# Performance work log

Hardware: AMD Instinct MI355X
Metric: run time of the kernel (lower is better)

The kernel has to match this reference:

```python
import jax, jax.numpy as jnp
import numpy as np

NUM_SEGMENTS = 64  # number of bags (max batch id + 1)
TEMP = 1.0
EPS_NORM = 1e-12
EPS_SOFTMAX = 1e-16

D = 1024
L = 128
N = 262144


def setup_inputs() -> dict:
    key = jax.random.key(0)
    ks = jax.random.split(key, 8)
    feature = jax.random.normal(ks[0], (N, D), dtype=jnp.float32)
    batch = jnp.sort(jax.random.randint(ks[1], (N,), 0, NUM_SEGMENTS, dtype=jnp.int32))
    # xavier_normal_ init: std = sqrt(2/(fan_in+fan_out))
    Wa = jax.random.normal(ks[2], (L, D), dtype=jnp.float32) * np.sqrt(2.0 / (D + L))
    ba = jnp.zeros((L,), dtype=jnp.float32)
    Wb = jax.random.normal(ks[3], (L, D), dtype=jnp.float32) * np.sqrt(2.0 / (D + L))
    bb = jnp.zeros((L,), dtype=jnp.float32)
    Wc = jax.random.normal(ks[4], (1, L), dtype=jnp.float32) * np.sqrt(2.0 / (L + 1))
    bc = jnp.zeros((1,), dtype=jnp.float32)
    return {"feature": feature, "batch": batch, "istrain": 0,
            "Wa": Wa, "ba": ba, "Wb": Wb, "bb": bb, "Wc": Wc, "bc": bc}


def segment_softmax(score, batch, num_segments):
    # score: [N, 1], batch: [N] segment ids (torch_geometric softmax semantics)
    seg_max = jax.ops.segment_max(score, batch, num_segments=num_segments)
    ex = jnp.exp(score - seg_max[batch])
    denom = jax.ops.segment_sum(ex, batch, num_segments=num_segments)
    return ex / (denom[batch] + EPS_SOFTMAX)


def reference(feature, batch, istrain, Wa, ba, Wb, bb, Wc, bc):
    # F.normalize: L2-normalize each row (dim=1)
    norm = jnp.linalg.norm(feature, axis=1, keepdims=True)
    instance_norm_feature = feature / jnp.maximum(norm, EPS_NORM)
    a = jax.nn.sigmoid(feature @ Wa.T + ba)          # [N, L]
    b = jnp.tanh(feature @ Wb.T + bb)                # [N, L]
    gated = a * b                                     # [N, L]
    score = (gated @ Wc.T + bc) / TEMP               # [N, 1]
    score = segment_softmax(score, batch, NUM_SEGMENTS)
    # istrain=0 -> dropout is identity in this reference
    return (instance_norm_feature, score)
```

## Files before the change

kernel.cpp:

```cpp
#include <hip/hip_runtime.h>

#define DD 1024
#define LL 128
#define NSEG 64
#define CHS 544
#define TB  17408
#define GRID 768
#define NTILE 16384

typedef float floatx4 __attribute__((ext_vector_type(4)));

__global__ __launch_bounds__(256)
void prep_kernel(const float* __restrict__ Wa, const float* __restrict__ Wb,
                 unsigned char* __restrict__ Wf8, float* __restrict__ denom,
                 float* __restrict__ score_raw)
{
    int gid = blockIdx.x * 256 + threadIdx.x;
    if (gid < 2 * LL * DD) {
        const int j    = gid & 7;
        const int lane = (gid >> 3) & 63;
        const int ct   = (gid >> 9) & 15;
        const int c    = gid >> 13;
        const int r = ct * 16 + (lane & 15);
        const int k = c * 32 + (lane >> 4) * 8 + j;
        const float v = ((r < LL) ? Wa[r * DD + k] : Wb[(r - LL) * DD + k]) * 16.0f;
        unsigned u = __builtin_amdgcn_cvt_pk_fp8_f32(v, v, 0, false);
        Wf8[gid] = (unsigned char)(u & 0xFF);
        score_raw[gid] = 0.0f;
    }
    if (gid < NSEG) denom[gid] = 0.0f;
}

__global__ __launch_bounds__(512, 6)
void fused_main(const float* __restrict__ feat,
                const unsigned char* __restrict__ Wf8,
                const float* __restrict__ ba,
                const float* __restrict__ bb,
                const float* __restrict__ Wc,
                float* __restrict__ out_norm,
                float* __restrict__ score_raw)
{
    __shared__ __align__(16) char tile[2 * TB];

    const int tid  = threadIdx.x;
    const int wave = tid >> 6;
    const int lane = tid & 63;
    const int s15  = lane & 15;
    const int l4   = lane >> 4;

    const float bav = ba[wave * 16 + s15];
    const float bbv = bb[wave * 16 + s15];
    const float wcv = Wc[wave * 16 + s15];
    const unsigned char* bb0 = Wf8 + (size_t)wave * 512 + (size_t)lane * 8;

    float4 L[2][4];

    auto issue = [&](long long T) {
        const float* fb = feat + ((size_t)T * 16 + wave * 2) * DD + lane * 4;
        #pragma unroll
        for (int i = 0; i < 2; ++i)
            #pragma unroll
            for (int c = 0; c < 4; ++c)
                L[i][c] = *reinterpret_cast<const float4*>(fb + (size_t)i * DD + c * 256);
    };

    long long t = blockIdx.x;
    int parity = 0;
    if (t < NTILE) issue(t);

    while (t < NTILE) {
        const long long row0 = t * 16;
        char* tb = tile + parity * TB;

        unsigned pw[2][4];
        #pragma unroll
        for (int i = 0; i < 2; ++i) {
            float ss = 0.0f;
            #pragma unroll
            for (int c = 0; c < 4; ++c)
                ss += L[i][c].x * L[i][c].x + L[i][c].y * L[i][c].y
                    + L[i][c].z * L[i][c].z + L[i][c].w * L[i][c].w;
            #pragma unroll
            for (int off = 32; off >= 1; off >>= 1) ss += __shfl_xor(ss, off);
            const float rinv = 1.0f / fmaxf(sqrtf(ss), 1e-12f);

            float* ob = out_norm + (row0 + wave * 2 + i) * DD + lane * 4;
            #pragma unroll
            for (int c = 0; c < 4; ++c) {
                float4 v;
                v.x = L[i][c].x * rinv; v.y = L[i][c].y * rinv;
                v.z = L[i][c].z * rinv; v.w = L[i][c].w * rinv;
                *reinterpret_cast<float4*>(ob + c * 256) = v;
            }
            #pragma unroll
            for (int c = 0; c < 4; ++c) {
                unsigned u = __builtin_amdgcn_cvt_pk_fp8_f32(L[i][c].x * 8.0f, L[i][c].y * 8.0f, 0, false);
                u = __builtin_amdgcn_cvt_pk_fp8_f32(L[i][c].z * 8.0f, L[i][c].w * 8.0f, u, true);
                pw[i][c] = u;
            }
        }

        #pragma unroll
        for (int i = 0; i < 2; ++i) {
            const int r = wave * 2 + i;
            #pragma unroll
            for (int c = 0; c < 4; ++c) {
                const int chunk = (lane >> 3) + c * 8;
                const int addr  = parity * TB + chunk * CHS + r * 32 + ((lane >> 1) & 3) * 8 + (lane & 1) * 4;
                *reinterpret_cast<unsigned*>(tile + addr) = pw[i][c];
            }
        }

        const long long tn = t + GRID;
        if (tn < NTILE) issue(tn);
        __builtin_amdgcn_sched_barrier(0);

        __syncthreads();

        floatx4 acc0 = (floatx4)0.0f;
        floatx4 acc1 = (floatx4)0.0f;
        #pragma unroll 4
        for (int c = 0; c < 32; ++c) {
            const long long a8 = *reinterpret_cast<const long long*>(tb + c * CHS + s15 * 32 + l4 * 8);
            const long long w0 = *reinterpret_cast<const long long*>(bb0 + (size_t)c * 8192);
            const long long w1 = *reinterpret_cast<const long long*>(bb0 + (size_t)c * 8192 + 4096);
            acc0 = __builtin_amdgcn_mfma_f32_16x16x32_fp8_fp8(a8, w0, acc0, 0, 0, 0);
            acc1 = __builtin_amdgcn_mfma_f32_16x16x32_fp8_fp8(a8, w1, acc1, 0, 0, 0);
        }

        {
            const float S = 1.0f / 128.0f;
            float s[4];
            #pragma unroll
            for (int j = 0; j < 4; ++j) {
                const float av = 1.0f / (1.0f + expf(-(acc0[j] * S + bav)));
                const float bv = tanhf(acc1[j] * S + bbv);
                s[j] = av * bv * wcv;
            }
            #pragma unroll
            for (int j = 0; j < 4; ++j) {
                s[j] += __shfl_xor(s[j], 1);
                s[j] += __shfl_xor(s[j], 2);
                s[j] += __shfl_xor(s[j], 4);
                s[j] += __shfl_xor(s[j], 8);
            }
            if (s15 == 0) {
                #pragma unroll
                for (int j = 0; j < 4; ++j)
                    atomicAdd(&score_raw[row0 + l4 * 4 + j], s[j]);
            }
        }

        t = tn;
        parity ^= 1;
    }
}

__global__ __launch_bounds__(256)
void seg_exp_kernel(float* __restrict__ score_inout, const int* __restrict__ batch,
                    float* __restrict__ denom, int n)
{
    __shared__ float sd[NSEG];
    const int t = threadIdx.x;
    if (t < NSEG) sd[t] = 0.0f;
    __syncthreads();
    const int stride = gridDim.x * blockDim.x;
    for (int i = blockIdx.x * blockDim.x + t; i < n; i += stride) {
        const float e = expf(score_inout[i]);
        score_inout[i] = e;
        atomicAdd(&sd[batch[i]], e);
    }
    __syncthreads();
    if (t < NSEG) atomicAdd(&denom[t], sd[t]);
}

__global__ __launch_bounds__(256)
void seg_div_kernel(float* __restrict__ score_inout, const int* __restrict__ batch,
                    const float* __restrict__ denom, int n)
{
    const int stride = gridDim.x * blockDim.x;
    for (int i = blockIdx.x * blockDim.x + threadIdx.x; i < n; i += stride)
        score_inout[i] = score_inout[i] / (denom[batch[i]] + 1e-16f);
}

extern "C" void kernel_launch(void* const* d_in, const int* in_sizes, int n_in,
                              void* d_out, int out_size, void* d_ws, size_t ws_size,
                              hipStream_t stream)
{
    const float* feat  = (const float*)d_in[0];
    const int*   batch = (const int*)d_in[1];
    const float* Wa = (const float*)d_in[3];
    const float* ba = (const float*)d_in[4];
    const float* Wb = (const float*)d_in[5];
    const float* bb = (const float*)d_in[6];
    const float* Wc = (const float*)d_in[7];

    const int N = in_sizes[1];

    float* out_norm  = (float*)d_out;
    float* out_score = (float*)d_out + (size_t)N * DD;

    char* ws = (char*)d_ws;
    unsigned char* Wf8 = (unsigned char*)ws;
    float* denom = (float*)(ws + 2 * LL * DD);

    prep_kernel<<<(2 * LL * DD + 255) / 256, 256, 0, stream>>>(Wa, Wb, Wf8, denom, out_score);
    fused_main<<<GRID, 512, 0, stream>>>(feat, Wf8, ba, bb, Wc, out_norm, out_score);
    seg_exp_kernel<<<512, 256, 0, stream>>>(out_score, batch, denom, N);
    seg_div_kernel<<<512, 256, 0, stream>>>(out_score, batch, denom, N);
}
```

Before: 546.4 us.

## Fuse segment softmax kernels with grid barrier, nontemporal loads, fast math

Merges the exp/sum and divide segment-softmax kernels into one launch that waits on a global atomic counter as a grid-wide barrier, removing one kernel launch. The main kernel now loads features with nontemporal hints and issues the next tile's loads before the LDS stores. It also swaps expf/tanhf for __expf-based sigmoid and tanh. The spin barrier relies on all 256 blocks being co-resident, and the exp-based tanh can overflow to inf/inf for large inputs.

```diff
diff --git a/kernel.cpp b/kernel.cpp
--- a/kernel.cpp
+++ b/kernel.cpp
@@ -7,13 +7,15 @@
 #define TB  17408
 #define GRID 768
 #define NTILE 16384
+#define SGRID 256
 
 typedef float floatx4 __attribute__((ext_vector_type(4)));
+typedef float f4v __attribute__((ext_vector_type(4)));
 
 __global__ __launch_bounds__(256)
 void prep_kernel(const float* __restrict__ Wa, const float* __restrict__ Wb,
                  unsigned char* __restrict__ Wf8, float* __restrict__ denom,
-                 float* __restrict__ score_raw)
+                 unsigned* __restrict__ counter, float* __restrict__ score_raw)
 {
     int gid = blockIdx.x * 256 + threadIdx.x;
     if (gid < 2 * LL * DD) {
@@ -29,6 +31,7 @@
         score_raw[gid] = 0.0f;
     }
     if (gid < NSEG) denom[gid] = 0.0f;
+    if (gid == NSEG) *counter = 0u;
 }
 
 __global__ __launch_bounds__(512, 6)
@@ -53,7 +56,7 @@
     const float wcv = Wc[wave * 16 + s15];
     const unsigned char* bb0 = Wf8 + (size_t)wave * 512 + (size_t)lane * 8;
 
-    float4 L[2][4];
+    f4v L[2][4];
 
     auto issue = [&](long long T) {
         const float* fb = feat + ((size_t)T * 16 + wave * 2) * DD + lane * 4;
@@ -61,7 +64,8 @@
         for (int i = 0; i < 2; ++i)
             #pragma unroll
             for (int c = 0; c < 4; ++c)
-                L[i][c] = *reinterpret_cast<const float4*>(fb + (size_t)i * DD + c * 256);
+                L[i][c] = __builtin_nontemporal_load(
+                    reinterpret_cast<const f4v*>(fb + (size_t)i * DD + c * 256));
     };
 
     long long t = blockIdx.x;
@@ -78,8 +82,8 @@
             float ss = 0.0f;
             #pragma unroll
             for (int c = 0; c < 4; ++c)
-                ss += L[i][c].x * L[i][c].x + L[i][c].y * L[i][c].y
-                    + L[i][c].z * L[i][c].z + L[i][c].w * L[i][c].w;
+                ss += L[i][c][0]*L[i][c][0] + L[i][c][1]*L[i][c][1]
+                    + L[i][c][2]*L[i][c][2] + L[i][c][3]*L[i][c][3];
             #pragma unroll
             for (int off = 32; off >= 1; off >>= 1) ss += __shfl_xor(ss, off);
             const float rinv = 1.0f / fmaxf(sqrtf(ss), 1e-12f);
@@ -87,18 +91,21 @@
             float* ob = out_norm + (row0 + wave * 2 + i) * DD + lane * 4;
             #pragma unroll
             for (int c = 0; c < 4; ++c) {
-                float4 v;
-                v.x = L[i][c].x * rinv; v.y = L[i][c].y * rinv;
-                v.z = L[i][c].z * rinv; v.w = L[i][c].w * rinv;
-                *reinterpret_cast<float4*>(ob + c * 256) = v;
+                f4v v;
+                v[0] = L[i][c][0] * rinv; v[1] = L[i][c][1] * rinv;
+                v[2] = L[i][c][2] * rinv; v[3] = L[i][c][3] * rinv;
+                *reinterpret_cast<f4v*>(ob + c * 256) = v;
             }
             #pragma unroll
             for (int c = 0; c < 4; ++c) {
-                unsigned u = __builtin_amdgcn_cvt_pk_fp8_f32(L[i][c].x * 8.0f, L[i][c].y * 8.0f, 0, false);
-                u = __builtin_amdgcn_cvt_pk_fp8_f32(L[i][c].z * 8.0f, L[i][c].w * 8.0f, u, true);
+                unsigned u = __builtin_amdgcn_cvt_pk_fp8_f32(L[i][c][0] * 8.0f, L[i][c][1] * 8.0f, 0, false);
+                u = __builtin_amdgcn_cvt_pk_fp8_f32(L[i][c][2] * 8.0f, L[i][c][3] * 8.0f, u, true);
                 pw[i][c] = u;
             }
         }
+
+        const long long tn = t + GRID;
+        if (tn < NTILE) issue(tn);
 
         #pragma unroll
         for (int i = 0; i < 2; ++i) {
@@ -110,9 +117,6 @@
                 *reinterpret_cast<unsigned*>(tile + addr) = pw[i][c];
             }
         }
-
-        const long long tn = t + GRID;
-        if (tn < NTILE) issue(tn);
         __builtin_amdgcn_sched_barrier(0);
 
         __syncthreads();
@@ -133,8 +137,11 @@
             float s[4];
             #pragma unroll
             for (int j = 0; j < 4; ++j) {
-                const float av = 1.0f / (1.0f + expf(-(acc0[j] * S + bav)));
-                const float bv = tanhf(acc1[j] * S + bbv);
+                const float xa = acc0[j] * S + bav;
+                const float xb = acc1[j] * S + bbv;
+                const float av = 1.0f / (1.0f + __expf(-xa));
+                const float eb = __expf(2.0f * xb);
+                const float bv = (eb - 1.0f) / (eb + 1.0f);
                 s[j] = av * bv * wcv;
             }
             #pragma unroll
@@ -157,30 +164,36 @@
 }
 
 __global__ __launch_bounds__(256)
-void seg_exp_kernel(float* __restrict__ score_inout, const int* __restrict__ batch,
-                    float* __restrict__ denom, int n)
+void seg_kernel(float* __restrict__ score_inout, const int* __restrict__ batch,
+                float* __restrict__ denom, unsigned* __restrict__ counter, int n)
 {
     __shared__ float sd[NSEG];
     const int t = threadIdx.x;
     if (t < NSEG) sd[t] = 0.0f;
     __syncthreads();
-    const int stride = gridDim.x * blockDim.x;
-    for (int i = blockIdx.x * blockDim.x + t; i < n; i += stride) {
+
+    const int stride = SGRID * 256;
+    for (int i = blockIdx.x * 256 + t; i < n; i += stride) {
         const float e = expf(score_inout[i]);
         score_inout[i] = e;
         atomicAdd(&sd[batch[i]], e);
     }
     __syncthreads();
     if (t < NSEG) atomicAdd(&denom[t], sd[t]);
-}
-
-__global__ __launch_bounds__(256)
-void seg_div_kernel(float* __restrict__ score_inout, const int* __restrict__ batch,
-                    const float* __restrict__ denom, int n)
-{
-    const int stride = gridDim.x * blockDim.x;
-    for (int i = blockIdx.x * blockDim.x + threadIdx.x; i < n; i += stride)
-        score_inout[i] = score_inout[i] / (denom[batch[i]] + 1e-16f);
+
+    __threadfence();
+    __syncthreads();
+    if (t == 0) {
+        atomicAdd(counter, 1u);
+        while (atomicAdd(counter, 0u) < SGRID) { __builtin_amdgcn_s_sleep(8); }
+    }
+    __syncthreads();
+
+    if (t < NSEG) sd[t] = atomicAdd(&denom[t], 0.0f);
+    __syncthreads();
+
+    for (int i = blockIdx.x * 256 + t; i < n; i += stride)
+        score_inout[i] = score_inout[i] / (sd[batch[i]] + 1e-16f);
 }
 
 extern "C" void kernel_launch(void* const* d_in, const int* in_sizes, int n_in,
@@ -202,10 +215,10 @@
 
     char* ws = (char*)d_ws;
     unsigned char* Wf8 = (unsigned char*)ws;
-    float* denom = (float*)(ws + 2 * LL * DD);
-
-    prep_kernel<<<(2 * LL * DD + 255) / 256, 256, 0, stream>>>(Wa, Wb, Wf8, denom, out_score);
+    float*    denom   = (float*)(ws + 2 * LL * DD);
+    unsigned* counter = (unsigned*)(ws + 2 * LL * DD + 256);
+
+    prep_kernel<<<(2 * LL * DD + 255) / 256, 256, 0, stream>>>(Wa, Wb, Wf8, denom, counter, out_score);
     fused_main<<<GRID, 512, 0, stream>>>(feat, Wf8, ba, bb, Wc, out_norm, out_score);
-    seg_exp_kernel<<<512, 256, 0, stream>>>(out_score, batch, denom, N);
-    seg_div_kernel<<<512, 256, 0, stream>>>(out_score, batch, denom, N);
-}
+    seg_kernel<<<SGRID, 256, 0, stream>>>(out_score, batch, denom, counter, N);
+}
```

Measured after the change: 590.4 us. 1.08x slower.
